# Kernel tuning notes

Measured on AMD Instinct MI355X. Metric: run time of the kernel, lower is better.

The kernel has to match this reference:

```python
import jax, jax.numpy as jnp
import numpy as np

CDIM = 256  # part_size for energy_pooling_mask


def setup_inputs() -> dict:
    key = jax.random.key(0)
    ks = jax.random.split(key, 6)
    B, T, IDIM, HDIM, ODIM = 8, 2048, 512, 2048, 512
    x = jax.random.normal(ks[0], (B, T, IDIM), dtype=jnp.float32)
    mask_prev = jax.random.randint(ks[1], (B, T, HDIM), 0, 2, dtype=jnp.int32)
    W_enc = jax.random.normal(ks[2], (HDIM, IDIM), dtype=jnp.float32) * 0.02
    b_enc = jax.random.normal(ks[3], (HDIM,), dtype=jnp.float32) * 0.02
    W_dec = jax.random.normal(ks[4], (ODIM, HDIM), dtype=jnp.float32) * 0.02
    b_dec = jax.random.normal(ks[5], (ODIM,), dtype=jnp.float32) * 0.02
    return {"x": x, "mask_prev": mask_prev, "W_enc": W_enc, "b_enc": b_enc,
            "W_dec": W_dec, "b_dec": b_dec}


def _energy_pooling_mask(h, part_size):
    # topk over channel (last) dim of h^2; share=True -> k = 2*part_size
    B, T, H = h.shape
    k2 = 2 * part_size
    _, idx = jax.lax.top_k(h * h, k2)            # [B, T, 2c] unique indices
    idx_f = idx.reshape(B * T, k2)
    rows = jnp.arange(B * T)[:, None]
    base = jnp.zeros((B * T, H), dtype=h.dtype)
    # sum of one-hots over unique indices == scatter-set of 1.0
    mask_share = base.at[rows, idx_f].set(1.0).reshape(B, T, H)
    mask_cur = base.at[rows, idx_f[:, :part_size]].set(1.0).reshape(B, T, H)
    return mask_cur, mask_share


def reference(x, mask_prev, W_enc, b_enc, W_dec, b_dec):
    # encoder: Linear(idim -> hdim)
    h = jnp.einsum('bti,hi->bth', x, W_enc) + b_enc
    # hidden_exclude_activation with mask_prev given:
    # h[mask_prev.bool()] = 0
    mp = mask_prev.astype(h.dtype)
    h = jnp.where(mp > 0, jnp.zeros((), h.dtype), h)
    mask_cur, mask_cur_share = _energy_pooling_mask(h, CDIM)
    mask_prev_new = mp + mask_cur
    # h.masked_fill(~mask_cur_share.bool(), 0)
    h = h * mask_cur_share
    # decoder_src: Linear(hdim -> odim)
    out = jnp.einsum('bth,oh->bto', h, W_dec) + b_dec
    return out, mask_prev_new
```

## Files before the change

kernel.cpp:

```cpp
#include <hip/hip_runtime.h>
#include <hip/hip_bf16.h>

typedef __attribute__((ext_vector_type(8))) __bf16 bf16x8;
typedef __attribute__((ext_vector_type(4))) float f32x4;

#define MDIM 16384
#define HDIM 2048
#define IDIM 512
#define ODIM 512
#define CAP 768

static __device__ __forceinline__ unsigned short f2bf(float f) {
  unsigned int u = __float_as_uint(f);
  unsigned int r = (u + 0x7fffu + ((u >> 16) & 1u)) >> 16;
  return (unsigned short)r;
}

__global__ void cvt_bf16_kernel(const float* __restrict__ src,
                                unsigned short* __restrict__ dst, int n) {
  int i = (blockIdx.x * 256 + threadIdx.x) * 4;
  if (i >= n) return;
  float4 v = *(const float4*)(src + i);
  unsigned int a = (unsigned int)f2bf(v.x) | ((unsigned int)f2bf(v.y) << 16);
  unsigned int b = (unsigned int)f2bf(v.z) | ((unsigned int)f2bf(v.w) << 16);
  uint2 st; st.x = a; st.y = b;
  *(uint2*)(dst + i) = st;
}

__global__ __launch_bounds__(256) void gemm1_kernel(
    const float* __restrict__ x,
    const float* __restrict__ wenc,
    const float* __restrict__ benc,
    float* __restrict__ h) {
  __shared__ __align__(16) float As[16][132];
  __shared__ __align__(16) float Bs[16][132];
  const int t = threadIdx.x;
  const int tx = t & 15, ty = t >> 4;
  const int m0 = blockIdx.y * 128;
  const int n0 = blockIdx.x * 128;
  const int r0 = t >> 2;
  const int k4 = (t & 3) * 4;

  const float* pa0 = x + (size_t)(m0 + r0) * IDIM + k4;
  const float* pa1 = x + (size_t)(m0 + 64 + r0) * IDIM + k4;
  const float* pb0 = wenc + (size_t)(n0 + r0) * IDIM + k4;
  const float* pb1 = wenc + (size_t)(n0 + 64 + r0) * IDIM + k4;

  float acc[8][8];
#pragma unroll
  for (int i = 0; i < 8; ++i)
#pragma unroll
    for (int j = 0; j < 8; ++j) acc[i][j] = 0.f;

  float4 a0 = *(const float4*)(pa0);
  float4 a1 = *(const float4*)(pa1);
  float4 b0 = *(const float4*)(pb0);
  float4 b1 = *(const float4*)(pb1);

  for (int kt = 0; kt < IDIM; kt += 16) {
    __syncthreads();
#pragma unroll
    for (int j = 0; j < 4; ++j) {
      As[k4 + j][r0]      = ((const float*)&a0)[j];
      As[k4 + j][64 + r0] = ((const float*)&a1)[j];
      Bs[k4 + j][r0]      = ((const float*)&b0)[j];
      Bs[k4 + j][64 + r0] = ((const float*)&b1)[j];
    }
    __syncthreads();
    if (kt + 16 < IDIM) {
      a0 = *(const float4*)(pa0 + kt + 16);
      a1 = *(const float4*)(pa1 + kt + 16);
      b0 = *(const float4*)(pb0 + kt + 16);
      b1 = *(const float4*)(pb1 + kt + 16);
    }
#pragma unroll
    for (int k = 0; k < 16; ++k) {
      float4 av0 = *(const float4*)&As[k][ty * 4];
      float4 av1 = *(const float4*)&As[k][64 + ty * 4];
      float4 bv0 = *(const float4*)&Bs[k][tx * 4];
      float4 bv1 = *(const float4*)&Bs[k][64 + tx * 4];
      float am[8] = {av0.x, av0.y, av0.z, av0.w, av1.x, av1.y, av1.z, av1.w};
      float bm[8] = {bv0.x, bv0.y, bv0.z, bv0.w, bv1.x, bv1.y, bv1.z, bv1.w};
#pragma unroll
      for (int i = 0; i < 8; ++i)
#pragma unroll
        for (int j = 0; j < 8; ++j) acc[i][j] += am[i] * bm[j];
    }
  }
  float4 be0 = *(const float4*)(benc + n0 + tx * 4);
  float4 be1 = *(const float4*)(benc + n0 + 64 + tx * 4);
  float bb[8] = {be0.x, be0.y, be0.z, be0.w, be1.x, be1.y, be1.z, be1.w};
#pragma unroll
  for (int i = 0; i < 8; ++i) {
    int m = m0 + ((i < 4) ? (ty * 4 + i) : (64 + ty * 4 + (i - 4)));
    float* hrow = h + (size_t)m * HDIM + n0;
    float4 s0 = {acc[i][0] + bb[0], acc[i][1] + bb[1], acc[i][2] + bb[2], acc[i][3] + bb[3]};
    float4 s1 = {acc[i][4] + bb[4], acc[i][5] + bb[5], acc[i][6] + bb[6], acc[i][7] + bb[7]};
    *(float4*)(hrow + tx * 4) = s0;
    *(float4*)(hrow + 64 + tx * 4) = s1;
  }
}

__global__ __launch_bounds__(256) void select_kernel(
    float* __restrict__ hbuf,
    const int* __restrict__ maskp,
    unsigned short* __restrict__ hs) {
  const int row = blockIdx.x;
  const int t = threadIdx.x;
  const int lane = t & 63;
  const int w = t >> 6;
  __shared__ int hist[4096];
  __shared__ unsigned int cand512[CAP];
  __shared__ unsigned int cand256[CAP];
  __shared__ int scal[16];
  __shared__ int n512, n256;

  float* hrow = hbuf + (size_t)row * HDIM;
  const int* mrow = maskp + (size_t)row * HDIM;
  float hv[8];
  *(float4*)&hv[0] = *(const float4*)(hrow + t * 8);
  *(float4*)&hv[4] = *(const float4*)(hrow + t * 8 + 4);
  int4 mp0 = *(const int4*)(mrow + t * 8);
  int4 mp1 = *(const int4*)(mrow + t * 8 + 4);
  int mm[8] = {mp0.x, mp0.y, mp0.z, mp0.w, mp1.x, mp1.y, mp1.z, mp1.w};
#pragma unroll
  for (int i = 0; i < 8; ++i) hv[i] = (mm[i] > 0) ? 0.f : hv[i];
  unsigned int key[8];
#pragma unroll
  for (int i = 0; i < 8; ++i) key[i] = __float_as_uint(hv[i] * hv[i]);

#pragma unroll
  for (int i = 0; i < 16; ++i) hist[t + i * 256] = 0;
  if (t == 0) {
    n512 = 0; n256 = 0;
    scal[0] = 0; scal[1] = 0x40000000;
    scal[2] = 0; scal[3] = 0x40000000;
  }
  __syncthreads();
#pragma unroll
  for (int i = 0; i < 8; ++i)
    if (key[i]) atomicAdd(&hist[key[i] >> 20], 1);
  __syncthreads();

  if (w == 0) {
    const int base = lane * 64;
    int s = 0;
#pragma unroll
    for (int i = 0; i < 64; i += 4) {
      int4 hh = *(const int4*)&hist[base + i];
      s += hh.x + hh.y + hh.z + hh.w;
    }
    int rs = s;
#pragma unroll
    for (int d = 1; d < 64; d <<= 1) {
      int o = __shfl_down(rs, d, 64);
      rs += (lane + d < 64) ? o : 0;
    }
    int c = rs - s;
    for (int i = 60; i >= 0; i -= 4) {
      int4 hh = *(const int4*)&hist[base + i];
      int q[4] = {hh.x, hh.y, hh.z, hh.w};
#pragma unroll
      for (int j = 3; j >= 0; --j) {
        int hc = q[j];
        if (c < 512 && c + hc >= 512) { scal[0] = base + i + j; scal[1] = 512 - c; }
        if (c < 256 && c + hc >= 256) { scal[2] = base + i + j; scal[3] = 256 - c; }
        c += hc;
      }
    }
  }
  __syncthreads();
  const int b512 = scal[0], b256 = scal[2];
#pragma unroll
  for (int i = 0; i < 8; ++i) {
    if (key[i]) {
      int bin = (int)(key[i] >> 20);
      if (bin == b512) { int p = atomicAdd(&n512, 1); if (p < CAP) cand512[p] = key[i]; }
      if (bin == b256) { int p = atomicAdd(&n256, 1); if (p < CAP) cand256[p] = key[i]; }
    }
  }
  __syncthreads();

  if (w < 2) {
    const unsigned int bb = (unsigned int)scal[w * 2];
    const int r = scal[w * 2 + 1];
    const unsigned int* cand = w ? cand256 : cand512;
    int C = w ? n256 : n512;
    C = (C < CAP) ? C : CAP;
    unsigned int v = 0;
    if (r <= C) {
      v = bb << 20;
      for (int bit = 19; bit >= 0; --bit) {
        unsigned int cth = v | (1u << bit);
        int cnt = 0;
        for (int p = lane; p < C; p += 64) cnt += (cand[p] >= cth) ? 1 : 0;
#pragma unroll
        for (int d = 1; d < 64; d <<= 1) cnt += __shfl_xor(cnt, d, 64);
        if (cnt >= r) v = cth;
      }
    }
    if (lane == 0) scal[4 + w] = (int)v;
  }
  __syncthreads();
  const unsigned int v512 = (unsigned int)scal[4];
  const unsigned int v256 = (unsigned int)scal[5];

  int g = 0;
#pragma unroll
  for (int i = 0; i < 8; ++i) {
    g += (key[i] > v512) ? 1 : 0;
    g += (key[i] > v256) ? (1 << 16) : 0;
  }
#pragma unroll
  for (int d = 1; d < 64; d <<= 1) g += __shfl_xor(g, d, 64);
  if (lane == 0) scal[8 + w] = g;
  __syncthreads();
  g = scal[8] + scal[9] + scal[10] + scal[11];
  const int r512 = 512 - (g & 0xffff);
  const int r256 = 256 - (g >> 16);

  int tc = 0;
#pragma unroll
  for (int i = 0; i < 8; ++i) {
    tc += (key[i] == v512) ? 1 : 0;
    tc += (key[i] == v256) ? (1 << 16) : 0;
  }
  int sc = tc;
#pragma unroll
  for (int d = 1; d < 64; d <<= 1) {
    int o = __shfl_up(sc, d, 64);
    if (lane >= d) sc += o;
  }
  if (lane == 63) scal[12 + w] = sc;
  __syncthreads();
  int excl = sc - tc;
  for (int i = 0; i < w; ++i) excl += scal[12 + i];
  int run512 = excl & 0xffff;
  int run256 = (excl >> 16) & 0xffff;

  float mpn[8];
  unsigned int hb[4];
#pragma unroll
  for (int i = 0; i < 8; ++i) {
    bool share, cur;
    if (key[i] > v512) share = true;
    else if (key[i] == v512) { share = (run512 < r512); run512++; }
    else share = false;
    if (key[i] > v256) cur = true;
    else if (key[i] == v256) { cur = (run256 < r256); run256++; }
    else cur = false;
    mpn[i] = (float)mm[i] + (cur ? 1.0f : 0.0f);
    unsigned short bbits = f2bf(share ? hv[i] : 0.0f);
    if (i & 1) hb[i >> 1] |= ((unsigned int)bbits << 16);
    else hb[i >> 1] = (unsigned int)bbits;
  }
  float4 s0 = {mpn[0], mpn[1], mpn[2], mpn[3]};
  float4 s1 = {mpn[4], mpn[5], mpn[6], mpn[7]};
  *(float4*)(hrow + t * 8) = s0;
  *(float4*)(hrow + t * 8 + 4) = s1;
  uint4 hstore = {hb[0], hb[1], hb[2], hb[3]};
  *(uint4*)(hs + (size_t)row * HDIM + t * 8) = hstore;
}

__global__ __launch_bounds__(256) void gemm2_kernel(
    const unsigned short* __restrict__ A,
    const unsigned short* __restrict__ B,
    const float* __restrict__ bdec,
    float* __restrict__ out) {
  __shared__ __align__(16) __bf16 As[128 * 32];
  __shared__ __align__(16) __bf16 Bs[128 * 32];
  const int t = threadIdx.x;
  const int lane = t & 63;
  const int w = t >> 6;
  const int wm = w >> 1, wn = w & 1;
  const int m0 = blockIdx.y * 128;
  const int n0 = blockIdx.x * 128;
  const int r = t >> 2;
  const int k8 = (t & 3) * 8;

  f32x4 acc[4][4];
#pragma unroll
  for (int i = 0; i < 4; ++i)
#pragma unroll
    for (int j = 0; j < 4; ++j) acc[i][j] = (f32x4){0.f, 0.f, 0.f, 0.f};

  const int la = lane & 15;
  const int kq = (lane >> 4) * 8;

  for (int kt = 0; kt < HDIM; kt += 32) {
    uint4 a0 = *(const uint4*)(A + (size_t)(m0 + r) * HDIM + kt + k8);
    uint4 a1 = *(const uint4*)(A + (size_t)(m0 + 64 + r) * HDIM + kt + k8);
    uint4 b0 = *(const uint4*)(B + (size_t)(n0 + r) * HDIM + kt + k8);
    uint4 b1 = *(const uint4*)(B + (size_t)(n0 + 64 + r) * HDIM + kt + k8);
    __syncthreads();
    *(uint4*)&As[r * 32 + k8] = a0;
    *(uint4*)&As[(64 + r) * 32 + k8] = a1;
    *(uint4*)&Bs[r * 32 + k8] = b0;
    *(uint4*)&Bs[(64 + r) * 32 + k8] = b1;
    __syncthreads();
    bf16x8 af[4], bg[4];
#pragma unroll
    for (int mi = 0; mi < 4; ++mi)
      af[mi] = *(const bf16x8*)&As[(wm * 64 + mi * 16 + la) * 32 + kq];
#pragma unroll
    for (int ni = 0; ni < 4; ++ni)
      bg[ni] = *(const bf16x8*)&Bs[(wn * 64 + ni * 16 + la) * 32 + kq];
#pragma unroll
    for (int mi = 0; mi < 4; ++mi)
#pragma unroll
      for (int ni = 0; ni < 4; ++ni)
        acc[mi][ni] = __builtin_amdgcn_mfma_f32_16x16x32_bf16(
            af[mi], bg[ni], acc[mi][ni], 0, 0, 0);
  }
  const int rq = (lane >> 4) * 4;
#pragma unroll
  for (int mi = 0; mi < 4; ++mi) {
#pragma unroll
    for (int ni = 0; ni < 4; ++ni) {
      int n = n0 + wn * 64 + ni * 16 + la;
      float bd = bdec[n];
#pragma unroll
      for (int rr = 0; rr < 4; ++rr) {
        int m = m0 + wm * 64 + mi * 16 + rq + rr;
        out[(size_t)m * ODIM + n] = acc[mi][ni][rr] + bd;
      }
    }
  }
}

extern "C" void kernel_launch(void* const* d_in, const int* in_sizes, int n_in,
                              void* d_out, int out_size, void* d_ws, size_t ws_size,
                              hipStream_t stream) {
  const float* x = (const float*)d_in[0];
  const int* mask_prev = (const int*)d_in[1];
  const float* W_enc = (const float*)d_in[2];
  const float* b_enc = (const float*)d_in[3];
  const float* W_dec = (const float*)d_in[4];
  const float* b_dec = (const float*)d_in[5];

  float* out = (float*)d_out;
  float* hbuf = out + (size_t)MDIM * ODIM;
  unsigned short* hs = (unsigned short*)d_ws;
  unsigned short* wdec = hs + (size_t)MDIM * HDIM;

  cvt_bf16_kernel<<<dim3((ODIM * HDIM) / (256 * 4)), dim3(256), 0, stream>>>(
      W_dec, wdec, ODIM * HDIM);
  gemm1_kernel<<<dim3(HDIM / 128, MDIM / 128), dim3(256), 0, stream>>>(
      x, W_enc, b_enc, hbuf);
  select_kernel<<<dim3(MDIM), dim3(256), 0, stream>>>(hbuf, mask_prev, hs);
  gemm2_kernel<<<dim3(ODIM / 128, MDIM / 128), dim3(256), 0, stream>>>(
      hs, wdec, b_dec, out);
}
```

Baseline: 855.9 us.

## Deepen gemm1 K-tile to 32 and halve gemm2 M-tile to 64

The fp32 encoder GEMM now stages 32-deep K tiles instead of 16. Each thread loads 16 contiguous floats per row, which halves the number of barrier pairs, but the register prefetch of the next tile is dropped. The bf16 decoder GEMM uses 64-row M tiles, which doubles the grid to 1024 blocks for more occupancy and parallelism on the small N dimension. The cost is that each B tile is reused less, and gemm1's loads are no longer overlapped with compute.

```diff
diff --git a/kernel.cpp b/kernel.cpp
--- a/kernel.cpp
+++ b/kernel.cpp
@@ -32,19 +32,17 @@
     const float* __restrict__ wenc,
     const float* __restrict__ benc,
     float* __restrict__ h) {
-  __shared__ __align__(16) float As[16][132];
-  __shared__ __align__(16) float Bs[16][132];
+  __shared__ __align__(16) float As[32][132];
+  __shared__ __align__(16) float Bs[32][132];
   const int t = threadIdx.x;
   const int tx = t & 15, ty = t >> 4;
   const int m0 = blockIdx.y * 128;
   const int n0 = blockIdx.x * 128;
-  const int r0 = t >> 2;
-  const int k4 = (t & 3) * 4;
-
-  const float* pa0 = x + (size_t)(m0 + r0) * IDIM + k4;
-  const float* pa1 = x + (size_t)(m0 + 64 + r0) * IDIM + k4;
-  const float* pb0 = wenc + (size_t)(n0 + r0) * IDIM + k4;
-  const float* pb1 = wenc + (size_t)(n0 + 64 + r0) * IDIM + k4;
+  const int r0 = t >> 1;
+  const int kh = (t & 1) * 16;
+
+  const float* pa = x + (size_t)(m0 + r0) * IDIM + kh;
+  const float* pb = wenc + (size_t)(n0 + r0) * IDIM + kh;
 
   float acc[8][8];
 #pragma unroll
@@ -52,29 +50,32 @@
 #pragma unroll
     for (int j = 0; j < 8; ++j) acc[i][j] = 0.f;
 
-  float4 a0 = *(const float4*)(pa0);
-  float4 a1 = *(const float4*)(pa1);
-  float4 b0 = *(const float4*)(pb0);
-  float4 b1 = *(const float4*)(pb1);
-
-  for (int kt = 0; kt < IDIM; kt += 16) {
+  for (int kt = 0; kt < IDIM; kt += 32) {
+    float4 a0 = *(const float4*)(pa + kt);
+    float4 a1 = *(const float4*)(pa + kt + 4);
+    float4 a2 = *(const float4*)(pa + kt + 8);
+    float4 a3 = *(const float4*)(pa + kt + 12);
+    float4 b0 = *(const float4*)(pb + kt);
+    float4 b1 = *(const float4*)(pb + kt + 4);
+    float4 b2 = *(const float4*)(pb + kt + 8);
+    float4 b3 = *(const float4*)(pb + kt + 12);
     __syncthreads();
-#pragma unroll
-    for (int j = 0; j < 4; ++j) {
-      As[k4 + j][r0]      = ((const float*)&a0)[j];
-      As[k4 + j][64 + r0] = ((const float*)&a1)[j];
-      Bs[k4 + j][r0]      = ((const float*)&b0)[j];
-      Bs[k4 + j][64 + r0] = ((const float*)&b1)[j];
+    {
+      const float* aa = (const float*)&a0;
+      const float av[16] = {a0.x, a0.y, a0.z, a0.w, a1.x, a1.y, a1.z, a1.w,
+                            a2.x, a2.y, a2.z, a2.w, a3.x, a3.y, a3.z, a3.w};
+      const float bv[16] = {b0.x, b0.y, b0.z, b0.w, b1.x, b1.y, b1.z, b1.w,
+                            b2.x, b2.y, b2.z, b2.w, b3.x, b3.y, b3.z, b3.w};
+      (void)aa;
+#pragma unroll
+      for (int j = 0; j < 16; ++j) {
+        As[kh + j][r0] = av[j];
+        Bs[kh + j][r0] = bv[j];
+      }
     }
     __syncthreads();
-    if (kt + 16 < IDIM) {
-      a0 = *(const float4*)(pa0 + kt + 16);
-      a1 = *(const float4*)(pa1 + kt + 16);
-      b0 = *(const float4*)(pb0 + kt + 16);
-      b1 = *(const float4*)(pb1 + kt + 16);
-    }
-#pragma unroll
-    for (int k = 0; k < 16; ++k) {
+#pragma unroll
+    for (int k = 0; k < 32; ++k) {
       float4 av0 = *(const float4*)&As[k][ty * 4];
       float4 av1 = *(const float4*)&As[k][64 + ty * 4];
       float4 bv0 = *(const float4*)&Bs[k][tx * 4];
@@ -267,20 +268,20 @@
     const unsigned short* __restrict__ B,
     const float* __restrict__ bdec,
     float* __restrict__ out) {
-  __shared__ __align__(16) __bf16 As[128 * 32];
+  __shared__ __align__(16) __bf16 As[64 * 32];
   __shared__ __align__(16) __bf16 Bs[128 * 32];
   const int t = threadIdx.x;
   const int lane = t & 63;
   const int w = t >> 6;
   const int wm = w >> 1, wn = w & 1;
-  const int m0 = blockIdx.y * 128;
+  const int m0 = blockIdx.y * 64;
   const int n0 = blockIdx.x * 128;
   const int r = t >> 2;
   const int k8 = (t & 3) * 8;
 
-  f32x4 acc[4][4];
-#pragma unroll
-  for (int i = 0; i < 4; ++i)
+  f32x4 acc[2][4];
+#pragma unroll
+  for (int i = 0; i < 2; ++i)
 #pragma unroll
     for (int j = 0; j < 4; ++j) acc[i][j] = (f32x4){0.f, 0.f, 0.f, 0.f};
 
@@ -289,24 +290,22 @@
 
   for (int kt = 0; kt < HDIM; kt += 32) {
     uint4 a0 = *(const uint4*)(A + (size_t)(m0 + r) * HDIM + kt + k8);
-    uint4 a1 = *(const uint4*)(A + (size_t)(m0 + 64 + r) * HDIM + kt + k8);
     uint4 b0 = *(const uint4*)(B + (size_t)(n0 + r) * HDIM + kt + k8);
     uint4 b1 = *(const uint4*)(B + (size_t)(n0 + 64 + r) * HDIM + kt + k8);
     __syncthreads();
     *(uint4*)&As[r * 32 + k8] = a0;
-    *(uint4*)&As[(64 + r) * 32 + k8] = a1;
     *(uint4*)&Bs[r * 32 + k8] = b0;
     *(uint4*)&Bs[(64 + r) * 32 + k8] = b1;
     __syncthreads();
-    bf16x8 af[4], bg[4];
-#pragma unroll
-    for (int mi = 0; mi < 4; ++mi)
-      af[mi] = *(const bf16x8*)&As[(wm * 64 + mi * 16 + la) * 32 + kq];
+    bf16x8 af[2], bg[4];
+#pragma unroll
+    for (int mi = 0; mi < 2; ++mi)
+      af[mi] = *(const bf16x8*)&As[(wm * 32 + mi * 16 + la) * 32 + kq];
 #pragma unroll
     for (int ni = 0; ni < 4; ++ni)
       bg[ni] = *(const bf16x8*)&Bs[(wn * 64 + ni * 16 + la) * 32 + kq];
 #pragma unroll
-    for (int mi = 0; mi < 4; ++mi)
+    for (int mi = 0; mi < 2; ++mi)
 #pragma unroll
       for (int ni = 0; ni < 4; ++ni)
         acc[mi][ni] = __builtin_amdgcn_mfma_f32_16x16x32_bf16(
@@ -314,14 +313,14 @@
   }
   const int rq = (lane >> 4) * 4;
 #pragma unroll
-  for (int mi = 0; mi < 4; ++mi) {
+  for (int mi = 0; mi < 2; ++mi) {
 #pragma unroll
     for (int ni = 0; ni < 4; ++ni) {
       int n = n0 + wn * 64 + ni * 16 + la;
       float bd = bdec[n];
 #pragma unroll
       for (int rr = 0; rr < 4; ++rr) {
-        int m = m0 + wm * 64 + mi * 16 + rq + rr;
+        int m = m0 + wm * 32 + mi * 16 + rq + rr;
         out[(size_t)m * ODIM + n] = acc[mi][ni][rr] + bd;
       }
     }
@@ -348,6 +347,6 @@
   gemm1_kernel<<<dim3(HDIM / 128, MDIM / 128), dim3(256), 0, stream>>>(
       x, W_enc, b_enc, hbuf);
   select_kernel<<<dim3(MDIM), dim3(256), 0, stream>>>(hbuf, mask_prev, hs);
-  gemm2_kernel<<<dim3(ODIM / 128, MDIM / 128), dim3(256), 0, stream>>>(
+  gemm2_kernel<<<dim3(ODIM / 128, MDIM / 64), dim3(256), 0, stream>>>(
       hs, wdec, b_dec, out);
 }
```

Result: faster. 837.7 us (-2.1%).
